# Kernel tuning notes

Measured on AMD Instinct MI355X. Metric: run time of the kernel, lower is better.

The kernel has to match this reference:

```python
import jax, jax.numpy as jnp
import numpy as np
from jax import lax

NMS_THRESHOLD = 0.7
POST_NMS_TOP_N = 1000
N_BOXES = 2048
CAP = 8  # max vertices of intersection of two convex quads
EPS = 1e-8


def _cross(a, b):
    return a[..., 0] * b[..., 1] - a[..., 1] * b[..., 0]


def _corners(b):
    # b: (5,) [xc, yc, w, h, theta] -> (4,2) CCW corners
    xc, yc, w, h, t = b[0], b[1], b[2], b[3], b[4]
    c, s = jnp.cos(t), jnp.sin(t)
    lx = jnp.array([-0.5, 0.5, 0.5, -0.5], dtype=b.dtype) * w
    ly = jnp.array([-0.5, -0.5, 0.5, 0.5], dtype=b.dtype) * h
    x = xc + lx * c - ly * s
    y = yc + lx * s + ly * c
    return jnp.stack([x, y], axis=-1)


def _clip(poly, n, p0, p1):
    # Sutherland-Hodgman clip of poly (CAP,2) with n valid verts against
    # half-plane to the left of edge p0->p1 (CCW interior).
    idx = jnp.arange(CAP)
    valid = idx < n
    nsafe = jnp.maximum(n, 1)
    prev = poly[(idx + nsafe - 1) % nsafe]
    e = p1 - p0
    d_cur = _cross(e, poly - p0)
    d_prev = _cross(e, prev - p0)
    cur_in = d_cur >= 0.0
    prev_in = d_prev >= 0.0
    denom = d_prev - d_cur
    denom = jnp.where(jnp.abs(denom) < EPS, EPS, denom)
    t = d_prev / denom
    ipt = prev + t[:, None] * (poly - prev)  # edge/half-plane intersection
    # per input vertex emit: [crossing point, current vertex]
    pts = jnp.stack([ipt, poly], axis=1).reshape(2 * CAP, 2)
    vmask = jnp.stack([valid & (cur_in != prev_in), valid & cur_in], axis=1).reshape(2 * CAP)
    order = jnp.argsort(~vmask, stable=True)  # compact valid points to front
    new_n = jnp.minimum(jnp.sum(vmask).astype(jnp.int32), CAP)
    return pts[order][:CAP], new_n


def _inter_area(b1, b2):
    poly = jnp.zeros((CAP, 2), dtype=b1.dtype).at[:4].set(_corners(b1))
    n = jnp.int32(4)
    r2 = _corners(b2)
    for k in range(4):
        poly, n = _clip(poly, n, r2[k], r2[(k + 1) % 4])
    idx = jnp.arange(CAP)
    valid = idx < n
    nxt = (idx + 1) % jnp.maximum(n, 1)
    area = 0.5 * jnp.abs(jnp.sum(jnp.where(valid, _cross(poly, poly[nxt]), 0.0)))
    return jnp.where(n >= 3, area, 0.0)


def _pairwise_iou(boxes):
    inter = jax.vmap(lambda b1: jax.vmap(lambda b2: _inter_area(b1, b2))(boxes))(boxes)
    area = boxes[:, 2] * boxes[:, 3]
    return inter / (area[:, None] + area[None, :] - inter + EPS)


def _greedy(iou, thresh, topn):
    n = iou.shape[0]
    js = jnp.arange(n, dtype=jnp.int32)

    def body(i, st):
        keep, cnt, sup = st
        take = jnp.logical_and(jnp.logical_not(sup[i]), cnt < topn)
        keep = jnp.where(take, keep.at[cnt].set(i), keep)
        sup = sup | (take & (iou[i] >= thresh) & (js > i))
        return keep, cnt + take.astype(jnp.int32), sup

    keep0 = jnp.full((topn,), -1, dtype=jnp.int32)
    keep, _, _ = lax.fori_loop(0, n, body, (keep0, jnp.int32(0), jnp.zeros((n,), dtype=bool)))
    return keep


def setup_inputs() -> dict:
    key = jax.random.key(0)
    k1, k2, k3 = jax.random.split(key, 3)
    xy = jax.random.uniform(k1, (N_BOXES, 2), minval=0.0, maxval=1024.0)
    wh = jax.random.uniform(k2, (N_BOXES, 2), minval=8.0, maxval=128.0)
    th = jax.random.uniform(k3, (N_BOXES, 1), minval=-np.pi / 2, maxval=np.pi / 2)
    r_boxes = jnp.concatenate([xy, wh, th], axis=1).astype(jnp.float32)
    return {"r_boxes": r_boxes}


def reference(r_boxes):
    # boxes assumed pre-sorted by score (as in the original module)
    iou = _pairwise_iou(r_boxes)
    keep = _greedy(iou, NMS_THRESHOLD, POST_NMS_TOP_N)  # (post_nms_top_n,), -1 padded
    return keep
```

## Files before the change

### kernel.cpp

```cpp
#include <hip/hip_runtime.h>
#include <hip/hip_bf16.h>

#define CAP 8
#define EPSF 1e-8f
#define NMS_THR 0.7f
#define TOPN 1000
#define ITILE 16
#define QCAP (256 * ITILE)
#define SQCAP 1024
#define CAPR 64
#define SCRATCH_ROWS 256
#define OVF_CAP 8192

__device__ __forceinline__ float rect_inter_area_cs(
    float xc1, float yc1, float w1, float h1, float c1, float s1,
    float xc2, float yc2, float w2, float h2, float c2, float s2)
{
    float px[CAP], py[CAP];
    {
        float lx0 = -0.5f * w1, lx1 = 0.5f * w1;
        float ly0 = -0.5f * h1, ly1 = 0.5f * h1;
        px[0] = xc1 + lx0 * c1 - ly0 * s1;  py[0] = yc1 + lx0 * s1 + ly0 * c1;
        px[1] = xc1 + lx1 * c1 - ly0 * s1;  py[1] = yc1 + lx1 * s1 + ly0 * c1;
        px[2] = xc1 + lx1 * c1 - ly1 * s1;  py[2] = yc1 + lx1 * s1 + ly1 * c1;
        px[3] = xc1 + lx0 * c1 - ly1 * s1;  py[3] = yc1 + lx0 * s1 + ly1 * c1;
#pragma unroll
        for (int s2i = 4; s2i < CAP; ++s2i) { px[s2i] = 0.f; py[s2i] = 0.f; }
    }
    float qx[4], qy[4];
    {
        float lx0 = -0.5f * w2, lx1 = 0.5f * w2;
        float ly0 = -0.5f * h2, ly1 = 0.5f * h2;
        qx[0] = xc2 + lx0 * c2 - ly0 * s2;  qy[0] = yc2 + lx0 * s2 + ly0 * c2;
        qx[1] = xc2 + lx1 * c2 - ly0 * s2;  qy[1] = yc2 + lx1 * s2 + ly0 * c2;
        qx[2] = xc2 + lx1 * c2 - ly1 * s2;  qy[2] = yc2 + lx1 * s2 + ly1 * c2;
        qx[3] = xc2 + lx0 * c2 - ly1 * s2;  qy[3] = yc2 + lx0 * s2 + ly1 * c2;
    }

    int n = 4;
#pragma unroll
    for (int e = 0; e < 4; ++e) {
        float p0x = qx[e], p0y = qy[e];
        float ex = qx[(e + 1) & 3] - p0x, ey = qy[(e + 1) & 3] - p0y;

        float pxp = px[0], pyp = py[0];
#pragma unroll
        for (int s = 1; s < CAP; ++s)
            if (s == n - 1) { pxp = px[s]; pyp = py[s]; }
        float dp = ex * (pyp - p0y) - ey * (pxp - p0x);

        float nx_[CAP], ny_[CAP];
#pragma unroll
        for (int s = 0; s < CAP; ++s) { nx_[s] = 0.f; ny_[s] = 0.f; }
        int m = 0;

#pragma unroll
        for (int k = 0; k < CAP; ++k) {
            bool act = (k < n);
            float pxc = px[k], pyc = py[k];
            float dc = ex * (pyc - p0y) - ey * (pxc - p0x);
            bool cin = (dc >= 0.0f), pin = (dp >= 0.0f);

            float den = dp - dc;
            den = (fabsf(den) < EPSF) ? EPSF : den;
            float t = dp / den;
            float ix = pxp + t * (pxc - pxp);
            float iy = pyp + t * (pyc - pyp);

            bool emit_cross = act && (cin != pin);
            if (emit_cross) {
#pragma unroll
                for (int s = 0; s < CAP; ++s)
                    if (s == m) { nx_[s] = ix; ny_[s] = iy; }
                ++m;
            }
            bool emit_cur = act && cin;
            if (emit_cur) {
#pragma unroll
                for (int s = 0; s < CAP; ++s)
                    if (s == m) { nx_[s] = pxc; ny_[s] = pyc; }
                ++m;
            }
            if (act) { pxp = pxc; pyp = pyc; dp = dc; }
        }
        n = (m < CAP) ? m : CAP;
#pragma unroll
        for (int s = 0; s < CAP; ++s) { px[s] = nx_[s]; py[s] = ny_[s]; }
    }

    if (n < 3) return 0.0f;
    float s = 0.0f;
#pragma unroll
    for (int k = 0; k < CAP; ++k) {
        if (k < n) {
            float nxk = px[(k + 1) & (CAP - 1)];
            float nyk = py[(k + 1) & (CAP - 1)];
            if (k == n - 1) { nxk = px[0]; nyk = py[0]; }
            s += px[k] * nyk - py[k] * nxk;
        }
    }
    return 0.5f * fabsf(s);
}

__device__ __forceinline__ unsigned long long rl64(unsigned long long v, int l) {
    unsigned int lo = (unsigned int)__builtin_amdgcn_readlane((int)(unsigned int)v, l);
    unsigned int hi = (unsigned int)__builtin_amdgcn_readlane((int)(v >> 32), l);
    return ((unsigned long long)hi << 32) | lo;
}

__global__ __launch_bounds__(256)
void filter_kernel(const float* __restrict__ boxes,
                   unsigned int* __restrict__ ctrs,
                   unsigned int* __restrict__ cnt_per_block,
                   unsigned int* __restrict__ pairs, int slice,
                   unsigned int* __restrict__ ovf_list, int n)
{
    __shared__ float4 atile[2 * ITILE];
    __shared__ unsigned int q[QCAP];
    __shared__ unsigned int sq[SQCAP];
    __shared__ int qcnt, scnt;

    const int tid = threadIdx.x;

    const int itiles = (n + ITILE - 1) / ITILE;
    const int jtiles = (n + 255) / 256;
    int L2 = blockIdx.x, jt = -1, it = 0;
    for (int q2 = 0; q2 < jtiles; ++q2) {
        int c2 = (q2 * 256 + 254) / ITILE + 1;
        c2 = (c2 < itiles) ? c2 : itiles;
        if (jt < 0) {
            if (L2 < c2) { jt = q2; it = L2; }
            else L2 -= c2;
        }
    }
    const int i0 = it * ITILE;
    const int j = jt * 256 + tid;

    if (tid == 0) { qcnt = 0; scnt = 0; }
    if (tid < ITILE) {
        int i = i0 + tid;
        if (i < n) {
            const float* b = boxes + (size_t)i * 5;
            float x = b[0], y = b[1], w = b[2], h = b[3], th = b[4];
            atile[2 * tid]     = make_float4(x, y, w, h);
            atile[2 * tid + 1] = make_float4(cosf(th), sinf(th),
                                             0.5f * sqrtf(w * w + h * h), w * h);
        } else {
            atile[2 * tid]     = make_float4(0.f, 0.f, 0.f, 0.f);
            atile[2 * tid + 1] = make_float4(0.f, 0.f, 0.f, 0.f);
        }
    }
    __syncthreads();

    float4 B0, B1;
    bool jok = (j < n);
    if (jok) {
        const float* b = boxes + (size_t)j * 5;
        float x = b[0], y = b[1], w = b[2], h = b[3], th = b[4];
        B0 = make_float4(x, y, w, h);
        B1 = make_float4(cosf(th), sinf(th),
                         0.5f * sqrtf(w * w + h * h), w * h);
    } else { B0 = make_float4(0,0,0,0); B1 = make_float4(0,0,0,0); }

#pragma unroll
    for (int ii = 0; ii < ITILE; ++ii) {
        int i = i0 + ii;
        float4 A0 = atile[2 * ii], A1 = atile[2 * ii + 1];
        bool pass = jok && (j > i) && (i < n);
        float dx = A0.x - B0.x, dy = A0.y - B0.y;
        float rr = A1.z + B1.z + 1e-2f;
        pass = pass && (dx * dx + dy * dy <= rr * rr);
        float amin = fminf(A1.w, B1.w), amax = fmaxf(A1.w, B1.w);
        pass = pass && (amin >= 0.699f * amax);
        if (pass) {
            int idx = atomicAdd(&qcnt, 1);
            q[idx] = ((unsigned int)ii << 16) | (unsigned int)j;
        }
    }
    __syncthreads();

    int qn = qcnt;
    for (int t = tid; t < qn; t += 256) {
        unsigned int pk = q[t];
        int ii = (int)(pk >> 16), j2 = (int)(pk & 0xffffu);
        int i2 = i0 + ii;
        float4 A0 = atile[2 * ii], A1 = atile[2 * ii + 1];
        const float* b = boxes + (size_t)j2 * 5;
        float x = b[0], y = b[1], w = b[2], h = b[3], th = b[4];
        float cj = cosf(th), sj = sinf(th);
        float a1 = A1.w, a2 = w * h;
        float inter = rect_inter_area_cs(A0.x, A0.y, A0.z, A0.w, A1.x, A1.y,
                                         x, y, w, h, cj, sj);
        float iou = inter / (a1 + a2 - inter + EPSF);
        if (iou >= NMS_THR) {
            unsigned int pr = ((unsigned int)i2 << 16) | (unsigned int)j2;
            int s2 = atomicAdd(&scnt, 1);
            if (s2 < SQCAP) sq[s2] = pr;
            else {
                unsigned int o = atomicAdd(&ctrs[1], 1u);
                if (o < OVF_CAP) ovf_list[o] = pr;
            }
        }
    }
    __syncthreads();

    int sn = (scnt < SQCAP) ? scnt : SQCAP;
    int wn = (sn < slice) ? sn : slice;
    for (int t = tid; t < wn; t += 256)
        pairs[(size_t)blockIdx.x * slice + t] = sq[t];
    for (int t = slice + tid; t < sn; t += 256) {
        unsigned int o = atomicAdd(&ctrs[1], 1u);
        if (o < OVF_CAP) ovf_list[o] = sq[t];
    }
    if (tid == 0) cnt_per_block[blockIdx.x] = (unsigned int)wn;
}

__global__ __launch_bounds__(256, 1)
void greedy_kernel(const unsigned int* __restrict__ ctrs,
                   const unsigned int* __restrict__ cnt_per_block,
                   const unsigned int* __restrict__ pairs, int slice,
                   const unsigned int* __restrict__ ovf_list,
                   unsigned int* __restrict__ scratch32,
                   int* __restrict__ keep, int n, int T)
{
    __shared__ unsigned int rowdat32[CAPR * 64];
    __shared__ unsigned int szv32[64];
    __shared__ int bexcl_lds[32];
    __shared__ int Rtot;

    const int tid = threadIdx.x;
    const int chunks = (n + 63) >> 6;

    for (int t = tid; t < 64; t += 256) szv32[t] = 0u;
    __syncthreads();

    for (int b = tid; b < T; b += 256) {
        int cb = (int)cnt_per_block[b];
        for (int t2 = 0; t2 < cb; ++t2) {
            unsigned int p = pairs[(size_t)b * slice + t2];
            int i = (int)(p >> 16);
            atomicOr(&szv32[((i >> 6) << 1) + ((i >> 5) & 1)], 1u << (i & 31));
        }
    }
    int ocnt = (int)ctrs[1]; if (ocnt > OVF_CAP) ocnt = OVF_CAP;
    for (int t = tid; t < ocnt; t += 256) {
        unsigned int p = ovf_list[t];
        int i = (int)(p >> 16);
        atomicOr(&szv32[((i >> 6) << 1) + ((i >> 5) & 1)], 1u << (i & 31));
    }
    __syncthreads();

    if (tid < 64) {
        int lane = tid;
        unsigned long long szv = (lane < chunks)
            ? ((unsigned long long)szv32[2 * lane] |
               ((unsigned long long)szv32[2 * lane + 1] << 32)) : 0ULL;
        int pc = __popcll(szv);
        int pref = pc;
#pragma unroll
        for (int d = 1; d < 64; d <<= 1) {
            int t = __shfl_up(pref, d);
            if (lane >= d) pref += t;
        }
        if (lane < chunks) bexcl_lds[lane] = pref - pc;
        if (lane == chunks - 1) Rtot = pref;
    }
    __syncthreads();

    int R = Rtot;
    int Rc = (R < CAPR) ? R : CAPR;
    int Rs = ((R < CAPR + SCRATCH_ROWS) ? R : (CAPR + SCRATCH_ROWS)) - Rc;
    for (int t = tid; t < Rc * 64; t += 256) rowdat32[t] = 0u;
    for (int t = tid; t < Rs * 64; t += 256) scratch32[t] = 0u;
    __syncthreads();

    for (int b = tid; b < T; b += 256) {
        int cb = (int)cnt_per_block[b];
        for (int t2 = 0; t2 < cb; ++t2) {
            unsigned int p = pairs[(size_t)b * slice + t2];
            int i = (int)(p >> 16), jj = (int)(p & 0xffffu);
            int c = i >> 6;
            unsigned long long szc =
                (unsigned long long)szv32[2 * c] |
                ((unsigned long long)szv32[2 * c + 1] << 32);
            int slot = bexcl_lds[c] +
                (int)__popcll(szc & (((i & 63) == 0) ? 0ULL
                                     : ((~0ULL) >> (64 - (i & 63)))));
            if (slot < CAPR)
                atomicOr(&rowdat32[slot * 64 + (jj >> 5)], 1u << (jj & 31));
            else if (slot < CAPR + SCRATCH_ROWS)
                atomicOr(&scratch32[(slot - CAPR) * 64 + (jj >> 5)],
                         1u << (jj & 31));
        }
    }
    for (int t = tid; t < ocnt; t += 256) {
        unsigned int p = ovf_list[t];
        int i = (int)(p >> 16), jj = (int)(p & 0xffffu);
        int c = i >> 6;
        unsigned long long szc =
            (unsigned long long)szv32[2 * c] |
            ((unsigned long long)szv32[2 * c + 1] << 32);
        int slot = bexcl_lds[c] +
            (int)__popcll(szc & (((i & 63) == 0) ? 0ULL
                                 : ((~0ULL) >> (64 - (i & 63)))));
        if (slot < CAPR)
            atomicOr(&rowdat32[slot * 64 + (jj >> 5)], 1u << (jj & 31));
        else if (slot < CAPR + SCRATCH_ROWS)
            atomicOr(&scratch32[(slot - CAPR) * 64 + (jj >> 5)],
                     1u << (jj & 31));
    }
    __syncthreads();

    if (tid >= 64) return;
    {
        const int lane = tid;
        unsigned long long szv = (lane < chunks)
            ? ((unsigned long long)szv32[2 * lane] |
               ((unsigned long long)szv32[2 * lane + 1] << 32)) : 0ULL;
        int base_excl = (lane < chunks) ? bexcl_lds[lane] : 0;

        auto rowread = [&](int slot, int word) -> unsigned long long {
            if (slot < CAPR)
                return (unsigned long long)rowdat32[slot * 64 + 2 * word] |
                       ((unsigned long long)rowdat32[slot * 64 + 2 * word + 1]
                        << 32);
            if (slot < CAPR + SCRATCH_ROWS)
                return (unsigned long long)
                           scratch32[(slot - CAPR) * 64 + 2 * word] |
                       ((unsigned long long)
                           scratch32[(slot - CAPR) * 64 + 2 * word + 1] << 32);
            return 0ULL;
        };

        unsigned long long acc = 0ULL;
        int cnt = 0;

        for (int c = 0; c < chunks; ++c) {
            if (cnt >= TOPN) break;
            const int base = c << 6;
            unsigned long long cw = rl64(acc, c);
            unsigned long long nzc = rl64(szv, c);
            unsigned long long valid =
                (n - base >= 64) ? ~0ULL : ((1ULL << (n - base)) - 1ULL);
            unsigned long long cand = ~cw & valid;
            int rem = TOPN - cnt;

            unsigned long long kmask;
            if ((nzc & cand) == 0ULL && __popcll(cand) <= rem) {
                kmask = cand;
            } else {
                int bexc = __builtin_amdgcn_readlane(base_excl, c);
                unsigned long long D = 0ULL;
                if ((nzc >> lane) & 1ULL) {
                    int slot = bexc +
                        (int)__popcll(nzc & ((lane == 0) ? 0ULL
                                             : ((~0ULL) >> (64 - lane))));
                    D = rowread(slot, c);
                }
                unsigned long long intra = __ballot((D & cand) != 0ULL);
                if ((intra & cand) == 0ULL && __popcll(cand) <= rem) {
                    kmask = cand;
                } else {
                    kmask = 0ULL;
                    int cl = cnt;
#pragma unroll
                    for (int k = 0; k < 64; ++k) {
                        if (!((cw >> k) & 1ULL) && cl < TOPN && (base + k) < n) {
                            cw |= rl64(D, k);
                            kmask |= (1ULL << k);
                            ++cl;
                        }
                    }
                }
            }

            if ((kmask >> lane) & 1ULL)
                keep[cnt + __popcll(kmask & ((1ULL << lane) - 1ULL))] =
                    base + lane;
            cnt += __popcll(kmask);

            unsigned long long orrows = kmask & nzc;
            if (orrows) {
                int bexc = __builtin_amdgcn_readlane(base_excl, c);
                while (orrows) {
                    int r = (int)__builtin_ctzll(orrows);
                    orrows &= orrows - 1ULL;
                    int slot = bexc +
                        (int)__popcll(nzc & ((r == 0) ? 0ULL
                                             : ((~0ULL) >> (64 - r))));
                    acc |= rowread(slot, lane & 31);
                }
            }
        }

        for (int t = cnt + lane; t < TOPN; t += 64) keep[t] = -1;
    }
}

extern "C" void kernel_launch(void* const* d_in, const int* in_sizes, int n_in,
                              void* d_out, int out_size, void* d_ws, size_t ws_size,
                              hipStream_t stream) {
    const float* boxes = (const float*)d_in[0];
    int n = in_sizes[0] / 5;
    int* keep = (int*)d_out;

    const int itiles = (n + ITILE - 1) / ITILE;
    const int jtiles = (n + 255) / 256;
    int T = 0;
    for (int q2 = 0; q2 < jtiles; ++q2) {
        int c2 = (q2 * 256 + 254) / ITILE + 1;
        T += (c2 < itiles) ? c2 : itiles;
    }

    unsigned int* ctrs = (unsigned int*)d_ws;
    unsigned int* cnt_per_block = ctrs + 4;
    size_t off_pairs = ((16 + (size_t)T * 4) + 15) & ~(size_t)15;
    size_t fixed_tail = (size_t)OVF_CAP * 4 + (size_t)SCRATCH_ROWS * 256 + 64;
    long avail = (long)ws_size - (long)off_pairs - (long)fixed_tail;
    int slice = (int)(avail / ((long)T * 4));
    if (slice > 256) slice = 256;
    if (slice < 16) slice = 16;
    unsigned int* pairs = (unsigned int*)((char*)d_ws + off_pairs);
    unsigned int* ovf_list = pairs + (size_t)T * slice;
    unsigned int* scratch32 = ovf_list + OVF_CAP;

    hipMemsetAsync(ctrs, 0, 16, stream);

    filter_kernel<<<T, 256, 0, stream>>>(boxes, ctrs, cnt_per_block, pairs,
                                         slice, ovf_list, n);
    greedy_kernel<<<1, 256, 0, stream>>>(ctrs, cnt_per_block, pairs, slice,
                                         ovf_list, scratch32, keep, n, T);
}
```

Baseline: 31.91 us.

## Enlarge i-tile, drop overflow list and memset, write pairs directly to global

```diff
diff --git a/kernel.cpp b/kernel.cpp
--- a/kernel.cpp
+++ b/kernel.cpp
@@ -5,12 +5,10 @@
 #define EPSF 1e-8f
 #define NMS_THR 0.7f
 #define TOPN 1000
-#define ITILE 16
-#define QCAP (256 * ITILE)
-#define SQCAP 1024
+#define ITILE 64
+#define QCAP 8192
 #define CAPR 64
-#define SCRATCH_ROWS 256
-#define OVF_CAP 8192
+#define SCRATCH_ROWS 512
 
 __device__ __forceinline__ float rect_inter_area_cs(
     float xc1, float yc1, float w1, float h1, float c1, float s1,
@@ -110,21 +108,19 @@
 
 __global__ __launch_bounds__(256)
 void filter_kernel(const float* __restrict__ boxes,
-                   unsigned int* __restrict__ ctrs,
                    unsigned int* __restrict__ cnt_per_block,
-                   unsigned int* __restrict__ pairs, int slice,
-                   unsigned int* __restrict__ ovf_list, int n)
+                   unsigned int* __restrict__ pairs, int slice, int n)
 {
     __shared__ float4 atile[2 * ITILE];
     __shared__ unsigned int q[QCAP];
-    __shared__ unsigned int sq[SQCAP];
     __shared__ int qcnt, scnt;
 
     const int tid = threadIdx.x;
+    const int bid = blockIdx.x;
 
     const int itiles = (n + ITILE - 1) / ITILE;
     const int jtiles = (n + 255) / 256;
-    int L2 = blockIdx.x, jt = -1, it = 0;
+    int L2 = bid, jt = -1, it = 0;
     for (int q2 = 0; q2 < jtiles; ++q2) {
         int c2 = (q2 * 256 + 254) / ITILE + 1;
         c2 = (c2 < itiles) ? c2 : itiles;
@@ -162,7 +158,6 @@
                          0.5f * sqrtf(w * w + h * h), w * h);
     } else { B0 = make_float4(0,0,0,0); B1 = make_float4(0,0,0,0); }
 
-#pragma unroll
     for (int ii = 0; ii < ITILE; ++ii) {
         int i = i0 + ii;
         float4 A0 = atile[2 * ii], A1 = atile[2 * ii + 1];
@@ -174,12 +169,26 @@
         pass = pass && (amin >= 0.699f * amax);
         if (pass) {
             int idx = atomicAdd(&qcnt, 1);
-            q[idx] = ((unsigned int)ii << 16) | (unsigned int)j;
-        }
-    }
-    __syncthreads();
-
-    int qn = qcnt;
+            if (idx < QCAP) {
+                q[idx] = ((unsigned int)ii << 16) | (unsigned int)j;
+            } else {
+                float a1 = A1.w, a2 = B1.w;
+                float inter = rect_inter_area_cs(
+                    A0.x, A0.y, A0.z, A0.w, A1.x, A1.y,
+                    B0.x, B0.y, B0.z, B0.w, B1.x, B1.y);
+                float iou = inter / (a1 + a2 - inter + EPSF);
+                if (iou >= NMS_THR) {
+                    int s2 = atomicAdd(&scnt, 1);
+                    if (s2 < slice)
+                        pairs[(size_t)bid * slice + s2] =
+                            ((unsigned int)i << 16) | (unsigned int)j;
+                }
+            }
+        }
+    }
+    __syncthreads();
+
+    int qn = (qcnt < QCAP) ? qcnt : QCAP;
     for (int t = tid; t < qn; t += 256) {
         unsigned int pk = q[t];
         int ii = (int)(pk >> 16), j2 = (int)(pk & 0xffffu);
@@ -193,33 +202,21 @@
                                          x, y, w, h, cj, sj);
         float iou = inter / (a1 + a2 - inter + EPSF);
         if (iou >= NMS_THR) {
-            unsigned int pr = ((unsigned int)i2 << 16) | (unsigned int)j2;
             int s2 = atomicAdd(&scnt, 1);
-            if (s2 < SQCAP) sq[s2] = pr;
-            else {
-                unsigned int o = atomicAdd(&ctrs[1], 1u);
-                if (o < OVF_CAP) ovf_list[o] = pr;
-            }
-        }
-    }
-    __syncthreads();
-
-    int sn = (scnt < SQCAP) ? scnt : SQCAP;
-    int wn = (sn < slice) ? sn : slice;
-    for (int t = tid; t < wn; t += 256)
-        pairs[(size_t)blockIdx.x * slice + t] = sq[t];
-    for (int t = slice + tid; t < sn; t += 256) {
-        unsigned int o = atomicAdd(&ctrs[1], 1u);
-        if (o < OVF_CAP) ovf_list[o] = sq[t];
-    }
-    if (tid == 0) cnt_per_block[blockIdx.x] = (unsigned int)wn;
+            if (s2 < slice)
+                pairs[(size_t)bid * slice + s2] =
+                    ((unsigned int)i2 << 16) | (unsigned int)j2;
+        }
+    }
+    __syncthreads();
+
+    if (tid == 0)
+        cnt_per_block[bid] = (unsigned int)((scnt < slice) ? scnt : slice);
 }
 
 __global__ __launch_bounds__(256, 1)
-void greedy_kernel(const unsigned int* __restrict__ ctrs,
-                   const unsigned int* __restrict__ cnt_per_block,
+void greedy_kernel(const unsigned int* __restrict__ cnt_per_block,
                    const unsigned int* __restrict__ pairs, int slice,
-                   const unsigned int* __restrict__ ovf_list,
                    unsigned int* __restrict__ scratch32,
                    int* __restrict__ keep, int n, int T)
 {
@@ -236,17 +233,12 @@
 
     for (int b = tid; b < T; b += 256) {
         int cb = (int)cnt_per_block[b];
+        if (cb > slice) cb = slice;
         for (int t2 = 0; t2 < cb; ++t2) {
             unsigned int p = pairs[(size_t)b * slice + t2];
             int i = (int)(p >> 16);
             atomicOr(&szv32[((i >> 6) << 1) + ((i >> 5) & 1)], 1u << (i & 31));
         }
-    }
-    int ocnt = (int)ctrs[1]; if (ocnt > OVF_CAP) ocnt = OVF_CAP;
-    for (int t = tid; t < ocnt; t += 256) {
-        unsigned int p = ovf_list[t];
-        int i = (int)(p >> 16);
-        atomicOr(&szv32[((i >> 6) << 1) + ((i >> 5) & 1)], 1u << (i & 31));
     }
     __syncthreads();
 
@@ -276,6 +268,7 @@
 
     for (int b = tid; b < T; b += 256) {
         int cb = (int)cnt_per_block[b];
+        if (cb > slice) cb = slice;
         for (int t2 = 0; t2 < cb; ++t2) {
             unsigned int p = pairs[(size_t)b * slice + t2];
             int i = (int)(p >> 16), jj = (int)(p & 0xffffu);
@@ -292,22 +285,6 @@
                 atomicOr(&scratch32[(slot - CAPR) * 64 + (jj >> 5)],
                          1u << (jj & 31));
         }
-    }
-    for (int t = tid; t < ocnt; t += 256) {
-        unsigned int p = ovf_list[t];
-        int i = (int)(p >> 16), jj = (int)(p & 0xffffu);
-        int c = i >> 6;
-        unsigned long long szc =
-            (unsigned long long)szv32[2 * c] |
-            ((unsigned long long)szv32[2 * c + 1] << 32);
-        int slot = bexcl_lds[c] +
-            (int)__popcll(szc & (((i & 63) == 0) ? 0ULL
-                                 : ((~0ULL) >> (64 - (i & 63)))));
-        if (slot < CAPR)
-            atomicOr(&rowdat32[slot * 64 + (jj >> 5)], 1u << (jj & 31));
-        else if (slot < CAPR + SCRATCH_ROWS)
-            atomicOr(&scratch32[(slot - CAPR) * 64 + (jj >> 5)],
-                     1u << (jj & 31));
     }
     __syncthreads();
 
@@ -412,22 +389,17 @@
         T += (c2 < itiles) ? c2 : itiles;
     }
 
-    unsigned int* ctrs = (unsigned int*)d_ws;
-    unsigned int* cnt_per_block = ctrs + 4;
-    size_t off_pairs = ((16 + (size_t)T * 4) + 15) & ~(size_t)15;
-    size_t fixed_tail = (size_t)OVF_CAP * 4 + (size_t)SCRATCH_ROWS * 256 + 64;
+    unsigned int* cnt_per_block = (unsigned int*)d_ws;
+    size_t off_pairs = (((size_t)T * 4) + 255) & ~(size_t)255;
+    size_t fixed_tail = (size_t)SCRATCH_ROWS * 256 + 256;
     long avail = (long)ws_size - (long)off_pairs - (long)fixed_tail;
-    int slice = (int)(avail / ((long)T * 4));
-    if (slice > 256) slice = 256;
-    if (slice < 16) slice = 16;
+    int slice = 256 * ITILE;
+    long maxslice = avail / ((long)T * 4);
+    if (slice > maxslice) slice = (int)maxslice;
     unsigned int* pairs = (unsigned int*)((char*)d_ws + off_pairs);
-    unsigned int* ovf_list = pairs + (size_t)T * slice;
-    unsigned int* scratch32 = ovf_list + OVF_CAP;
-
-    hipMemsetAsync(ctrs, 0, 16, stream);
-
-    filter_kernel<<<T, 256, 0, stream>>>(boxes, ctrs, cnt_per_block, pairs,
-                                         slice, ovf_list, n);
-    greedy_kernel<<<1, 256, 0, stream>>>(ctrs, cnt_per_block, pairs, slice,
-                                         ovf_list, scratch32, keep, n, T);
+    unsigned int* scratch32 = pairs + (size_t)T * slice;
+
+    filter_kernel<<<T, 256, 0, stream>>>(boxes, cnt_per_block, pairs, slice, n);
+    greedy_kernel<<<1, 256, 0, stream>>>(cnt_per_block, pairs, slice,
+                                         scratch32, keep, n, T);
 }
```

New measurement: 33.72 us. +5.7%, slower.
